# Kernel tuning notes

Hardware: AMD Instinct MI355X
Metric: run time of the kernel (lower is better)

Reference implementation:

```python
import jax, jax.numpy as jnp
import numpy as np

N = 30000      # nodes
E = 480000     # edges (before self-loops)
G = 30         # graphs
DIN = 256      # input_dim
DH = 64        # hidden_dim (per-head out channels)
H = 8          # heads in layers 0,1; last layer has 1 head


def _glorot(key, shape):
    fan_in, fan_out = shape[0], shape[-1]
    s = jnp.sqrt(2.0 / (fan_in + fan_out))
    return jax.random.normal(key, shape, dtype=jnp.float32) * s


def setup_inputs() -> dict:
    key = jax.random.key(0)
    ks = jax.random.split(key, 32)
    inp = {
        'x': jax.random.normal(ks[0], (N, DIN), dtype=jnp.float32),
        'edge_index': jax.random.randint(ks[1], (2, E), 0, N, dtype=jnp.int64),
        'batch': jnp.sort(jax.random.randint(ks[2], (N,), 0, G, dtype=jnp.int64)),
        # GAT layer 0: in=256 -> 8 heads x 64
        'W0': _glorot(ks[3], (DIN, H * DH)),
        'as0': _glorot(ks[4], (H, DH)), 'ad0': _glorot(ks[5], (H, DH)),
        'b0': jnp.zeros((H * DH,), jnp.float32),
        # GAT layer 1: in=512 -> 8 heads x 64
        'W1': _glorot(ks[6], (H * DH, H * DH)),
        'as1': _glorot(ks[7], (H, DH)), 'ad1': _glorot(ks[8], (H, DH)),
        'b1': jnp.zeros((H * DH,), jnp.float32),
        # GAT layer 2: in=512 -> 1 head x 64
        'W2': _glorot(ks[9], (H * DH, DH)),
        'as2': _glorot(ks[10], (1, DH)), 'ad2': _glorot(ks[11], (1, DH)),
        'b2': jnp.zeros((DH,), jnp.float32),
        # batch norms (feature sizes match actual activations)
        'bn0_g': jnp.ones((H * DH,), jnp.float32), 'bn0_b': jnp.zeros((H * DH,), jnp.float32),
        'bn1_g': jnp.ones((H * DH,), jnp.float32), 'bn1_b': jnp.zeros((H * DH,), jnp.float32),
        'bn2_g': jnp.ones((DH,), jnp.float32), 'bn2_b': jnp.zeros((DH,), jnp.float32),
        'ln_g': jnp.ones((DH,), jnp.float32), 'ln_b': jnp.zeros((DH,), jnp.float32),
        'fc1_w': _glorot(ks[12], (DH, DH // 2)), 'fc1_b': jnp.zeros((DH // 2,), jnp.float32),
        'fc2_w': _glorot(ks[13], (DH // 2, 2)), 'fc2_b': jnp.zeros((2,), jnp.float32),
    }
    return inp


def _gat(x, src, dst, W, a_src, a_dst, bias, heads):
    # x: [N, Fin]; project to [N, heads, DH]
    h = (x @ W).reshape(N, heads, DH)
    s_src = jnp.sum(h * a_src, axis=-1)  # [N, heads]
    s_dst = jnp.sum(h * a_dst, axis=-1)  # [N, heads]
    e = jax.nn.leaky_relu(s_src[src] + s_dst[dst], 0.2)  # [Etot, heads]
    # segment softmax over edges grouped by destination node
    m = jax.ops.segment_max(e, dst, num_segments=N)
    p = jnp.exp(e - m[dst])
    denom = jax.ops.segment_sum(p, dst, num_segments=N)
    alpha = p / (denom[dst] + 1e-16)
    out = jax.ops.segment_sum(h[src] * alpha[:, :, None], dst, num_segments=N)
    return out.reshape(N, heads * DH) + bias


def _bn(x, g, b):
    m = jnp.mean(x, axis=0)
    v = jnp.var(x, axis=0)
    return (x - m) / jnp.sqrt(v + 1e-5) * g + b


def _forward(x, edge_index, batch,
             W0, as0, ad0, b0, W1, as1, ad1, b1, W2, as2, ad2, b2,
             bn0_g, bn0_b, bn1_g, bn1_b, bn2_g, bn2_b,
             ln_g, ln_b, fc1_w, fc1_b, fc2_w, fc2_b):
    loops = jnp.arange(N, dtype=edge_index.dtype)
    src = jnp.concatenate([edge_index[0], loops])
    dst = jnp.concatenate([edge_index[1], loops])
    # layer 0: 256 -> 512; no residual (dim mismatch)
    x1 = jax.nn.elu(_bn(_gat(x, src, dst, W0, as0, ad0, b0, H), bn0_g, bn0_b))
    # layer 1: 512 -> 512; residual
    x2 = jax.nn.elu(_bn(_gat(x1, src, dst, W1, as1, ad1, b1, H), bn1_g, bn1_b)) + x1
    # layer 2 (single head): 512 -> 64; no residual
    x3 = jax.nn.elu(_bn(_gat(x2, src, dst, W2, as2, ad2, b2, 1), bn2_g, bn2_b))
    # layer norm
    mu = jnp.mean(x3, axis=-1, keepdims=True)
    var = jnp.var(x3, axis=-1, keepdims=True)
    xl = (x3 - mu) / jnp.sqrt(var + 1e-5) * ln_g + ln_b
    # global mean pool over graphs
    sums = jax.ops.segment_sum(xl, batch, num_segments=G)
    cnt = jax.ops.segment_sum(jnp.ones((N, 1), xl.dtype), batch, num_segments=G)
    pooled = sums / jnp.maximum(cnt, 1.0)
    hdd = jax.nn.elu(pooled @ fc1_w + fc1_b)
    logits = hdd @ fc2_w + fc2_b
    return jax.nn.log_softmax(logits, axis=1)


def reference(x, edge_index, batch,
              W0, as0, ad0, b0, W1, as1, ad1, b1, W2, as2, ad2, b2,
              bn0_g, bn0_b, bn1_g, bn1_b, bn2_g, bn2_b,
              ln_g, ln_b, fc1_w, fc1_b, fc2_w, fc2_b):
    return _forward(x, edge_index, batch,
                    W0, as0, ad0, b0, W1, as1, ad1, b1, W2, as2, ad2, b2,
                    bn0_g, bn0_b, bn1_g, bn1_b, bn2_g, bn2_b,
                    ln_g, ln_b, fc1_w, fc1_b, fc2_w, fc2_b)
```

## Files before the change

kernel.cpp:

```cpp
#include <hip/hip_runtime.h>
#include <math.h>

#define NODES 30000
#define NEDGE 480000
#define ETOT  (NODES + NEDGE)
#define NGRAPH 30
#define DIN 256
#define DH 64
#define CAP 128

typedef __bf16 bf16x8 __attribute__((ext_vector_type(8)));
typedef float  f32x4  __attribute__((ext_vector_type(4)));

static __device__ __forceinline__ float elu_f(float x){ return x > 0.f ? x : expm1f(x); }
static __device__ __forceinline__ float bf_lo(unsigned v){ return __uint_as_float(v << 16); }
static __device__ __forceinline__ float bf_hi(unsigned v){ return __uint_as_float(v & 0xffff0000u); }
static __device__ __forceinline__ unsigned pack_bf2(float a, float b){
  __bf16 ob[2] = {(__bf16)a, (__bf16)b};
  return *(unsigned*)ob;
}

__global__ void k_count(const int* __restrict__ ei, int* __restrict__ deg){
  int e = blockIdx.x*256 + threadIdx.x;
  if (e >= ETOT) return;
  int dst = (e < NEDGE) ? ei[NEDGE + e] : (e - NEDGE);
  atomicAdd(&deg[dst], 1);
}

__global__ void k_scan(const int* __restrict__ deg, int* __restrict__ rowptr){
  __shared__ int s[1024];
  int t = threadIdx.x;
  const int CH = (NODES + 1023) / 1024;
  int base = t * CH;
  int local = 0;
  for (int i = 0; i < CH; i++){ int idx = base + i; if (idx < NODES) local += deg[idx]; }
  s[t] = local; __syncthreads();
  for (int off = 1; off < 1024; off <<= 1){
    int v = (t >= off) ? s[t - off] : 0;
    __syncthreads();
    s[t] += v;
    __syncthreads();
  }
  int run = s[t] - local;
  for (int i = 0; i < CH; i++){
    int idx = base + i;
    if (idx < NODES){ rowptr[idx] = run; run += deg[idx]; }
  }
  if (t == 1023) rowptr[NODES] = s[1023];
}

__global__ void k_fill(const int* __restrict__ ei, const int* __restrict__ rowptr,
                       int* __restrict__ cursor, int* __restrict__ colA){
  int e = blockIdx.x*256 + threadIdx.x;
  if (e >= ETOT) return;
  int src, dst;
  if (e < NEDGE){ src = ei[e]; dst = ei[NEDGE + e]; }
  else          { src = e - NEDGE; dst = src; }
  int pos = atomicAdd(&cursor[dst], 1);
  colA[rowptr[dst] + pos] = src;
}

__global__ void k_cast4(const float* __restrict__ in, __bf16* __restrict__ out, int n4){
  int i = blockIdx.x*256 + threadIdx.x;
  if (i >= n4) return;
  float4 v = ((const float4*)in)[i];
  __bf16 o[4] = {(__bf16)v.x, (__bf16)v.y, (__bf16)v.z, (__bf16)v.w};
  *(uint2*)(out + (size_t)i*4) = *(const uint2*)o;
}

#define TW0 (512*256)
#define TW1 (512*512)
#define TW2 (64*512)
__global__ void k_transW_all(const float* __restrict__ W0, const float* __restrict__ W1,
                             const float* __restrict__ W2, __bf16* __restrict__ Wt0,
                             __bf16* __restrict__ Wt1, __bf16* __restrict__ Wt2){
  int idx = blockIdx.x*256 + threadIdx.x;
  if (idx < TW0){
    int n = idx >> 8, k = idx & 255;
    Wt0[idx] = (__bf16)W0[(size_t)k*512 + n];
  } else if (idx < TW0 + TW1){
    int j = idx - TW0;
    int n = j >> 9, k = j & 511;
    Wt1[j] = (__bf16)W1[(size_t)k*512 + n];
  } else if (idx < TW0 + TW1 + TW2){
    int j = idx - TW0 - TW1;
    int n = j >> 9, k = j & 511;
    Wt2[j] = (__bf16)W2[(size_t)k*64 + n];
  }
}

#define LSTR 72
__global__ __launch_bounds__(256) void k_gemm_bf16(const __bf16* __restrict__ A,
    const __bf16* __restrict__ Bt, __bf16* __restrict__ C,
    const float* __restrict__ asrc, const float* __restrict__ adst,
    float* __restrict__ ssrc, float* __restrict__ sdst, int heads,
    int M, int N, int K){
  __shared__ __align__(16) __bf16 As[128*LSTR];
  __shared__ __align__(16) __bf16 Bs[128*LSTR];
  int tid  = threadIdx.x;
  int lane = tid & 63, wave = tid >> 6;
  int wr = wave >> 1, wc = wave & 1;
  int q = lane >> 4, r = lane & 15;
  int rowBase = blockIdx.y * 128, colBase = blockIdx.x * 128;
  f32x4 acc[4][4] = {};
  for (int k0 = 0; k0 < K; k0 += 64){
    #pragma unroll
    for (int p = 0; p < 4; p++){
      int lin = p*256 + tid;
      int rr = lin >> 3, ko = (lin & 7) * 8;
      uint4 va = make_uint4(0,0,0,0);
      int gr = rowBase + rr;
      if (gr < M) va = *(const uint4*)(A + (size_t)gr*K + k0 + ko);
      *(uint4*)(&As[rr*LSTR + ko]) = va;
      uint4 vb = make_uint4(0,0,0,0);
      int gn = colBase + rr;
      if (gn < N) vb = *(const uint4*)(Bt + (size_t)gn*K + k0 + ko);
      *(uint4*)(&Bs[rr*LSTR + ko]) = vb;
    }
    __syncthreads();
    #pragma unroll
    for (int kk = 0; kk < 2; kk++){
      bf16x8 af[4], bfr[4];
      #pragma unroll
      for (int i = 0; i < 4; i++) af[i]  = *(const bf16x8*)(&As[(wr*64 + i*16 + r)*LSTR + kk*32 + q*8]);
      #pragma unroll
      for (int j = 0; j < 4; j++) bfr[j] = *(const bf16x8*)(&Bs[(wc*64 + j*16 + r)*LSTR + kk*32 + q*8]);
      #pragma unroll
      for (int i = 0; i < 4; i++)
        #pragma unroll
        for (int j = 0; j < 4; j++)
          acc[i][j] = __builtin_amdgcn_mfma_f32_16x16x32_bf16(af[i], bfr[j], acc[i][j], 0, 0, 0);
    }
    __syncthreads();
  }
  #pragma unroll
  for (int i = 0; i < 4; i++){
    #pragma unroll
    for (int j = 0; j < 4; j++){
      int col = colBase + wc*64 + j*16 + r;
      if (col >= N) continue;
      #pragma unroll
      for (int v = 0; v < 4; v++){
        int row = rowBase + wr*64 + i*16 + q*4 + v;
        if (row < M) C[(size_t)row*N + col] = (__bf16)acc[i][j][v];
      }
    }
  }
  int colW = colBase + wc*64;
  if (colW < N){
    int hb = colW >> 6;
    float a_s[4], a_d[4];
    #pragma unroll
    for (int j = 0; j < 4; j++){
      a_s[j] = asrc[hb*64 + j*16 + r];
      a_d[j] = adst[hb*64 + j*16 + r];
    }
    #pragma unroll
    for (int i = 0; i < 4; i++){
      #pragma unroll
      for (int v = 0; v < 4; v++){
        float s1 = 0.f, s2 = 0.f;
        #pragma unroll
        for (int j = 0; j < 4; j++){
          float av = acc[i][j][v];
          s1 += av * a_s[j];
          s2 += av * a_d[j];
        }
        #pragma unroll
        for (int off = 1; off < 16; off <<= 1){
          s1 += __shfl_xor(s1, off, 64);
          s2 += __shfl_xor(s2, off, 64);
        }
        if (r == 0){
          int row = rowBase + wr*64 + i*16 + q*4 + v;
          if (row < M){
            ssrc[(size_t)row*heads + hb] = s1;
            sdst[(size_t)row*heads + hb] = s2;
          }
        }
      }
    }
  }
}

__global__ __launch_bounds__(256) void k_gatagg8(const __bf16* __restrict__ hb,
    const float* __restrict__ ssrc, const float* __restrict__ sdst,
    const int* __restrict__ rowptr, const int* __restrict__ colA,
    const float* __restrict__ bias, __bf16* __restrict__ outb){
  int n = blockIdx.x;
  int t = threadIdx.x;
  __shared__ int ecol[CAP];
  __shared__ float p[CAP][9];
  __shared__ float dhv[8], sdsh[8], mh[8];
  int base = rowptr[n];
  int deg = rowptr[n+1] - base;
  if (t < 8) sdsh[t] = sdst[(size_t)n*8 + t];
  __syncthreads();
  int g = t >> 5, l = t & 31;
  if (deg <= CAP){
    if (t < deg){
      int c = colA[base + t];
      ecol[t] = c;
      const float4* sp = (const float4*)(ssrc + (size_t)c*8);
      float4 s0 = sp[0], s1 = sp[1];
      float v;
      v = s0.x + sdsh[0]; p[t][0] = v > 0.f ? v : 0.2f*v;
      v = s0.y + sdsh[1]; p[t][1] = v > 0.f ? v : 0.2f*v;
      v = s0.z + sdsh[2]; p[t][2] = v > 0.f ? v : 0.2f*v;
      v = s0.w + sdsh[3]; p[t][3] = v > 0.f ? v : 0.2f*v;
      v = s1.x + sdsh[4]; p[t][4] = v > 0.f ? v : 0.2f*v;
      v = s1.y + sdsh[5]; p[t][5] = v > 0.f ? v : 0.2f*v;
      v = s1.z + sdsh[6]; p[t][6] = v > 0.f ? v : 0.2f*v;
      v = s1.w + sdsh[7]; p[t][7] = v > 0.f ? v : 0.2f*v;
    }
    __syncthreads();
    {
      float m = -1e30f;
      for (int e = l; e < deg; e += 32) m = fmaxf(m, p[e][g]);
      #pragma unroll
      for (int off = 1; off < 32; off <<= 1) m = fmaxf(m, __shfl_xor(m, off, 64));
      float d = 0.f;
      for (int e = l; e < deg; e += 32){ float xv = __expf(p[e][g] - m); p[e][g] = xv; d += xv; }
      #pragma unroll
      for (int off = 1; off < 32; off <<= 1) d += __shfl_xor(d, off, 64);
      if (l == 0) dhv[g] = 1.f / (d + 1e-16f);
    }
    __syncthreads();
    int hh = g;
    float rcp = dhv[hh];
    float a0 = 0.f, a1 = 0.f, b0 = 0.f, b1 = 0.f;
    int e = 0;
    for (; e + 4 <= deg; e += 4){
      int c0 = ecol[e], c1 = ecol[e+1], c2 = ecol[e+2], c3 = ecol[e+3];
      float p0 = p[e][hh], p1 = p[e+1][hh], p2 = p[e+2][hh], p3 = p[e+3][hh];
      unsigned v0 = *(const unsigned*)(hb + (size_t)c0*512 + t*2);
      unsigned v1 = *(const unsigned*)(hb + (size_t)c1*512 + t*2);
      unsigned v2 = *(const unsigned*)(hb + (size_t)c2*512 + t*2);
      unsigned v3 = *(const unsigned*)(hb + (size_t)c3*512 + t*2);
      a0 += p0*bf_lo(v0); a1 += p0*bf_hi(v0);
      b0 += p1*bf_lo(v1); b1 += p1*bf_hi(v1);
      a0 += p2*bf_lo(v2); a1 += p2*bf_hi(v2);
      b0 += p3*bf_lo(v3); b1 += p3*bf_hi(v3);
    }
    for (; e < deg; e++){
      int c = ecol[e];
      float pe = p[e][hh];
      unsigned v = *(const unsigned*)(hb + (size_t)c*512 + t*2);
      a0 += pe*bf_lo(v); a1 += pe*bf_hi(v);
    }
    a0 += b0; a1 += b1;
    float o0 = a0*rcp + bias[t*2], o1 = a1*rcp + bias[t*2+1];
    *(unsigned*)(outb + (size_t)n*512 + t*2) = pack_bf2(o0, o1);
  } else {
    float m = -1e30f;
    for (int e = l; e < deg; e += 32){
      int c = colA[base + e];
      float sc = ssrc[(size_t)c*8 + g] + sdsh[g];
      sc = sc > 0.f ? sc : 0.2f*sc;
      m = fmaxf(m, sc);
    }
    #pragma unroll
    for (int off = 1; off < 32; off <<= 1) m = fmaxf(m, __shfl_xor(m, off, 64));
    if (l == 0) mh[g] = m;
    __syncthreads();
    float d = 0.f;
    float mm = mh[g];
    for (int e = l; e < deg; e += 32){
      int c = colA[base + e];
      float sc = ssrc[(size_t)c*8 + g] + sdsh[g];
      sc = sc > 0.f ? sc : 0.2f*sc;
      d += __expf(sc - mm);
    }
    #pragma unroll
    for (int off = 1; off < 32; off <<= 1) d += __shfl_xor(d, off, 64);
    if (l == 0) dhv[g] = 1.f / (d + 1e-16f);
    __syncthreads();
    int hh = g;
    float rcp = dhv[hh];
    float mhh = mh[hh];
    float a0 = 0.f, a1 = 0.f;
    for (int e = 0; e < deg; e++){
      int c = colA[base + e];
      float sc = ssrc[(size_t)c*8 + hh] + sdsh[hh];
      sc = sc > 0.f ? sc : 0.2f*sc;
      float pe = __expf(sc - mhh);
      unsigned v = *(const unsigned*)(hb + (size_t)c*512 + t*2);
      a0 += pe*bf_lo(v); a1 += pe*bf_hi(v);
    }
    float o0 = a0*rcp + bias[t*2], o1 = a1*rcp + bias[t*2+1];
    *(unsigned*)(outb + (size_t)n*512 + t*2) = pack_bf2(o0, o1);
  }
}

__global__ __launch_bounds__(256) void k_gatagg1(const __bf16* __restrict__ hb,
    const float* __restrict__ ssrc, const float* __restrict__ sdst,
    const int* __restrict__ rowptr, const int* __restrict__ colA,
    const float* __restrict__ bias, __bf16* __restrict__ outb){
  int n = blockIdx.x;
  int t = threadIdx.x;
  __shared__ int ecol[CAP];
  __shared__ float p[CAP];
  __shared__ float racc[8][64];
  __shared__ float dhv1, mh1, sds;
  int base = rowptr[n];
  int deg = rowptr[n+1] - base;
  if (t == 0) sds = sdst[n];
  __syncthreads();
  int g = t >> 5, l = t & 31;
  if (deg <= CAP){
    if (t < deg){
      int c = colA[base + t];
      ecol[t] = c;
      float sc = ssrc[c] + sds;
      p[t] = sc > 0.f ? sc : 0.2f*sc;
    }
    __syncthreads();
    if (t < 64){
      float m = -1e30f;
      for (int e = t; e < deg; e += 64) m = fmaxf(m, p[e]);
      #pragma unroll
      for (int off = 1; off < 64; off <<= 1) m = fmaxf(m, __shfl_xor(m, off, 64));
      float d = 0.f;
      for (int e = t; e < deg; e += 64){ float xv = __expf(p[e] - m); p[e] = xv; d += xv; }
      #pragma unroll
      for (int off = 1; off < 64; off <<= 1) d += __shfl_xor(d, off, 64);
      if (t == 0) dhv1 = 1.f / (d + 1e-16f);
    }
    __syncthreads();
    float a0 = 0.f, a1 = 0.f;
    for (int e = g; e < deg; e += 8){
      float pe = p[e];
      unsigned v = *(const unsigned*)(hb + (size_t)ecol[e]*64 + l*2);
      a0 += pe*bf_lo(v); a1 += pe*bf_hi(v);
    }
    racc[g][l*2] = a0; racc[g][l*2+1] = a1;
    __syncthreads();
    if (t < 32){
      float s0 = 0.f, s1 = 0.f;
      #pragma unroll
      for (int g2 = 0; g2 < 8; g2++){ s0 += racc[g2][t*2]; s1 += racc[g2][t*2+1]; }
      float rcp = dhv1;
      float o0 = s0*rcp + bias[t*2], o1 = s1*rcp + bias[t*2+1];
      *(unsigned*)(outb + (size_t)n*64 + t*2) = pack_bf2(o0, o1);
    }
  } else {
    if (t < 64){
      float m = -1e30f;
      for (int e = t; e < deg; e += 64){
        int c = colA[base + e];
        float sc = ssrc[c] + sds;
        sc = sc > 0.f ? sc : 0.2f*sc;
        m = fmaxf(m, sc);
      }
      #pragma unroll
      for (int off = 1; off < 64; off <<= 1) m = fmaxf(m, __shfl_xor(m, off, 64));
      if (t == 0) mh1 = m;
    }
    __syncthreads();
    if (t < 64){
      float d = 0.f;
      for (int e = t; e < deg; e += 64){
        int c = colA[base + e];
        float sc = ssrc[c] + sds;
        sc = sc > 0.f ? sc : 0.2f*sc;
        d += __expf(sc - mh1);
      }
      #pragma unroll
      for (int off = 1; off < 64; off <<= 1) d += __shfl_xor(d, off, 64);
      if (t == 0) dhv1 = 1.f / (d + 1e-16f);
    }
    __syncthreads();
    float a0 = 0.f, a1 = 0.f;
    float mm = mh1;
    for (int e = g; e < deg; e += 8){
      int c = colA[base + e];
      float sc = ssrc[c] + sds;
      sc = sc > 0.f ? sc : 0.2f*sc;
      float pe = __expf(sc - mm);
      unsigned v = *(const unsigned*)(hb + (size_t)c*64 + l*2);
      a0 += pe*bf_lo(v); a1 += pe*bf_hi(v);
    }
    racc[g][l*2] = a0; racc[g][l*2+1] = a1;
    __syncthreads();
    if (t < 32){
      float s0 = 0.f, s1 = 0.f;
      #pragma unroll
      for (int g2 = 0; g2 < 8; g2++){ s0 += racc[g2][t*2]; s1 += racc[g2][t*2+1]; }
      float rcp = dhv1;
      float o0 = s0*rcp + bias[t*2], o1 = s1*rcp + bias[t*2+1];
      *(unsigned*)(outb + (size_t)n*64 + t*2) = pack_bf2(o0, o1);
    }
  }
}

__global__ __launch_bounds__(256) void k_bnstat1(const __bf16* __restrict__ xb,
    float* __restrict__ partial, int F){
  int t = threadIdx.x;
  int OCT = F >> 3;
  int RPB = 256 / OCT;
  int o = t & (OCT - 1), r = t / OCT;
  int NB = gridDim.x;
  float s[8] = {}, q[8] = {};
  int step = NB * RPB;
  for (int n = blockIdx.x*RPB + r; n < NODES; n += step){
    uint4 v = *(const uint4*)(xb + (size_t)n*F + o*8);
    unsigned vv[4] = {v.x, v.y, v.z, v.w};
    #pragma unroll
    for (int j = 0; j < 4; j++){
      float lo = bf_lo(vv[j]), hi = bf_hi(vv[j]);
      s[2*j]   += lo; q[2*j]   += lo*lo;
      s[2*j+1] += hi; q[2*j+1] += hi*hi;
    }
  }
  __shared__ float red[256][17];
  #pragma unroll
  for (int j = 0; j < 8; j++){ red[t][j] = s[j]; red[t][8+j] = q[j]; }
  __syncthreads();
  for (int st = RPB >> 1; st > 0; st >>= 1){
    if (r < st){
      #pragma unroll
      for (int j = 0; j < 16; j++) red[t][j] += red[t + st*OCT][j];
    }
    __syncthreads();
  }
  if (r == 0){
    #pragma unroll
    for (int j = 0; j < 8; j++){
      partial[(size_t)(o*8 + j)*NB + blockIdx.x]     = red[t][j];
      partial[(size_t)(F + o*8 + j)*NB + blockIdx.x] = red[t][8 + j];
    }
  }
}

__global__ void k_bnstat2(const float* __restrict__ partial, float* __restrict__ sum,
                          float* __restrict__ sumsq, int F, int NB){
  int row = blockIdx.x;
  int t = threadIdx.x;
  float a = 0.f;
  for (int i = t; i < NB; i += 64) a += partial[(size_t)row*NB + i];
  #pragma unroll
  for (int off = 1; off < 64; off <<= 1) a += __shfl_xor(a, off, 64);
  if (t == 0){
    if (row < F) sum[row] = a;
    else         sumsq[row - F] = a;
  }
}

__global__ __launch_bounds__(256) void k_bnapply_b(const __bf16* __restrict__ xb,
    const float* __restrict__ sum, const float* __restrict__ sumsq,
    const float* __restrict__ g, const float* __restrict__ b,
    const __bf16* __restrict__ res, __bf16* __restrict__ y, int rows){
  int t = threadIdx.x;
  float2 sm = *(const float2*)(sum + t*2);
  float2 sq = *(const float2*)(sumsq + t*2);
  float2 gg = *(const float2*)(g + t*2);
  float2 bb = *(const float2*)(b + t*2);
  const float inv_n = 1.f / (float)NODES;
  float m0 = sm.x*inv_n, m1 = sm.y*inv_n;
  float v0 = sq.x*inv_n - m0*m0, v1 = sq.y*inv_n - m1*m1;
  float sc0 = gg.x * rsqrtf(v0 + 1e-5f), sc1 = gg.y * rsqrtf(v1 + 1e-5f);
  float sh0 = bb.x - m0*sc0, sh1 = bb.y - m1*sc1;
  int n0 = blockIdx.x * rows;
  for (int r = 0; r < rows; r++){
    int n = n0 + r;
    if (n >= NODES) break;
    size_t off = (size_t)n*512 + t*2;
    unsigned v = *(const unsigned*)(xb + off);
    float o0 = elu_f(bf_lo(v)*sc0 + sh0);
    float o1 = elu_f(bf_hi(v)*sc1 + sh1);
    if (res){
      unsigned rv = *(const unsigned*)(res + off);
      o0 += bf_lo(rv); o1 += bf_hi(rv);
    }
    *(unsigned*)(y + off) = pack_bf2(o0, o1);
  }
}

__global__ void k_bn_elu_ln_b(const __bf16* __restrict__ xb, const float* __restrict__ sum,
    const float* __restrict__ sumsq, const float* __restrict__ g, const float* __restrict__ b,
    const float* __restrict__ lg, const float* __restrict__ lb, float* __restrict__ y){
  int t = threadIdx.x;
  int l = t & 31, sub = t >> 5;
  int n = blockIdx.x*8 + sub;
  float2 sm = *(const float2*)(sum + l*2);
  float2 sq = *(const float2*)(sumsq + l*2);
  float2 gg = *(const float2*)(g + l*2);
  float2 bb = *(const float2*)(b + l*2);
  const float inv_n = 1.f / (float)NODES;
  float m0 = sm.x*inv_n, m1 = sm.y*inv_n;
  float va0 = sq.x*inv_n - m0*m0, va1 = sq.y*inv_n - m1*m1;
  float sc0 = gg.x * rsqrtf(va0 + 1e-5f), sc1 = gg.y * rsqrtf(va1 + 1e-5f);
  float sh0 = bb.x - m0*sc0, sh1 = bb.y - m1*sc1;
  unsigned v = *(const unsigned*)(xb + (size_t)n*64 + l*2);
  float x0 = elu_f(bf_lo(v)*sc0 + sh0);
  float x1 = elu_f(bf_hi(v)*sc1 + sh1);
  float s = x0 + x1;
  #pragma unroll
  for (int off = 1; off < 32; off <<= 1) s += __shfl_xor(s, off, 64);
  float mean = s * (1.f/64.f);
  float d0 = x0 - mean, d1 = x1 - mean;
  float qq = d0*d0 + d1*d1;
  #pragma unroll
  for (int off = 1; off < 32; off <<= 1) qq += __shfl_xor(qq, off, 64);
  float var = qq * (1.f/64.f);
  float inv = rsqrtf(var + 1e-5f);
  float2 o = make_float2(d0*inv*lg[l*2] + lb[l*2], d1*inv*lg[l*2+1] + lb[l*2+1]);
  *(float2*)(y + (size_t)n*64 + l*2) = o;
}

static __device__ int lbound(const int* a, int n, int v){
  int lo = 0, hi = n;
  while (lo < hi){ int mid = (lo + hi) >> 1; if (a[mid] < v) lo = mid + 1; else hi = mid; }
  return lo;
}

__global__ void k_pool(const float* __restrict__ xl, const int* __restrict__ batch,
                       float* __restrict__ pooled){
  int g = blockIdx.x;
  int t = threadIdx.x;
  int lo = lbound(batch, NODES, g);
  int hi = lbound(batch, NODES, g+1);
  int f = t & 63, grp = t >> 6;
  float acc = 0.f;
  for (int n = lo + grp; n < hi; n += 4) acc += xl[(size_t)n*DH + f];
  __shared__ float red[4][64];
  red[grp][f] = acc;
  __syncthreads();
  if (grp == 0){
    float s = red[0][f] + red[1][f] + red[2][f] + red[3][f];
    int cnt = hi - lo;
    pooled[g*DH + f] = s / fmaxf((float)cnt, 1.f);
  }
}

__global__ void k_head(const float* __restrict__ pooled, const float* __restrict__ w1,
                       const float* __restrict__ b1, const float* __restrict__ w2,
                       const float* __restrict__ b2, float* __restrict__ out){
  int g = threadIdx.x;
  if (g >= NGRAPH) return;
  const float* pd = pooled + g*DH;
  float hdd[32];
  for (int j = 0; j < 32; j++){
    float s = b1[j];
    for (int d = 0; d < DH; d++) s += pd[d]*w1[d*32 + j];
    hdd[j] = elu_f(s);
  }
  float l0 = b2[0], l1 = b2[1];
  for (int j = 0; j < 32; j++){ l0 += hdd[j]*w2[j*2]; l1 += hdd[j]*w2[j*2 + 1]; }
  float m = fmaxf(l0, l1);
  float lse = m + logf(expf(l0 - m) + expf(l1 - m));
  out[g*2]     = l0 - lse;
  out[g*2 + 1] = l1 - lse;
}

extern "C" void kernel_launch(void* const* d_in, const int* in_sizes, int n_in,
                              void* d_out, int out_size, void* d_ws, size_t ws_size,
                              hipStream_t stream){
  const float* x    = (const float*)d_in[0];
  const int*   ei   = (const int*)d_in[1];
  const int*   batch= (const int*)d_in[2];
  const float* W0   = (const float*)d_in[3];
  const float* as0  = (const float*)d_in[4];
  const float* ad0  = (const float*)d_in[5];
  const float* b0   = (const float*)d_in[6];
  const float* W1   = (const float*)d_in[7];
  const float* as1  = (const float*)d_in[8];
  const float* ad1  = (const float*)d_in[9];
  const float* b1   = (const float*)d_in[10];
  const float* W2   = (const float*)d_in[11];
  const float* as2  = (const float*)d_in[12];
  const float* ad2  = (const float*)d_in[13];
  const float* b2   = (const float*)d_in[14];
  const float* bn0g = (const float*)d_in[15];
  const float* bn0b = (const float*)d_in[16];
  const float* bn1g = (const float*)d_in[17];
  const float* bn1b = (const float*)d_in[18];
  const float* bn2g = (const float*)d_in[19];
  const float* bn2b = (const float*)d_in[20];
  const float* lng  = (const float*)d_in[21];
  const float* lnb  = (const float*)d_in[22];
  const float* fc1w = (const float*)d_in[23];
  const float* fc1b = (const float*)d_in[24];
  const float* fc2w = (const float*)d_in[25];
  const float* fc2b = (const float*)d_in[26];
  float* out = (float*)d_out;

  char* w = (char*)d_ws;
  auto alloc = [&](size_t bytes) -> char* {
    char* p = w; w += (bytes + 255) & ~(size_t)255; return p;
  };
  __bf16* xb0   = (__bf16*)alloc((size_t)NODES*DIN*2);
  __bf16* hbuf  = (__bf16*)alloc((size_t)NODES*512*2);
  __bf16* gbuf  = (__bf16*)alloc((size_t)NODES*512*2);
  __bf16* x1b   = (__bf16*)alloc((size_t)NODES*512*2);
  __bf16* x2b   = (__bf16*)alloc((size_t)NODES*512*2);
  __bf16* Wt0   = (__bf16*)alloc((size_t)TW0*2);
  __bf16* Wt1   = (__bf16*)alloc((size_t)TW1*2);
  __bf16* Wt2   = (__bf16*)alloc((size_t)TW2*2);
  float*  ssrc  = (float*)alloc((size_t)NODES*8*4);
  float*  sdst  = (float*)alloc((size_t)NODES*8*4);
  float*  xl    = (float*)alloc((size_t)NODES*DH*4);
  float*  pooled= (float*)alloc(NGRAPH*DH*4);
  int*    rowptr= (int*)alloc((NODES+1)*4);
  int*    colA  = (int*)alloc((size_t)ETOT*4);
  float*  partial=(float*)alloc((size_t)2*512*512*4);
  float*  sum0  = (float*)alloc(512*4);
  float*  sq0   = (float*)alloc(512*4);
  float*  sum1  = (float*)alloc(512*4);
  float*  sq1   = (float*)alloc(512*4);
  float*  sum2  = (float*)alloc(64*4);
  float*  sq2   = (float*)alloc(64*4);
  char* zbase  = w;
  int*   deg   = (int*)alloc(NODES*4);
  int*   cursor= (int*)alloc(NODES*4);
  size_t zbytes = (size_t)(w - zbase);
  hipMemsetAsync(zbase, 0, zbytes, stream);

  const int eb = (ETOT + 255)/256;
  k_count<<<eb, 256, 0, stream>>>(ei, deg);
  k_scan<<<1, 1024, 0, stream>>>(deg, rowptr);
  k_fill<<<eb, 256, 0, stream>>>(ei, rowptr, cursor, colA);

  k_cast4<<<(NODES*DIN/4 + 255)/256, 256, 0, stream>>>(x, xb0, NODES*DIN/4);
  k_transW_all<<<(TW0+TW1+TW2 + 255)/256, 256, 0, stream>>>(W0, W1, W2, Wt0, Wt1, Wt2);

  const int mb128 = (NODES + 127)/128;
  const int nb8 = (NODES + 7)/8;

  k_gemm_bf16<<<dim3(4, mb128), 256, 0, stream>>>(xb0, Wt0, hbuf, as0, ad0, ssrc, sdst, 8, NODES, 512, DIN);
  k_gatagg8<<<NODES, 256, 0, stream>>>(hbuf, ssrc, sdst, rowptr, colA, b0, gbuf);
  k_bnstat1<<<512, 256, 0, stream>>>(gbuf, partial, 512);
  k_bnstat2<<<1024, 64, 0, stream>>>(partial, sum0, sq0, 512, 512);
  k_bnapply_b<<<nb8, 256, 0, stream>>>(gbuf, sum0, sq0, bn0g, bn0b, nullptr, x1b, 8);

  k_gemm_bf16<<<dim3(4, mb128), 256, 0, stream>>>(x1b, Wt1, hbuf, as1, ad1, ssrc, sdst, 8, NODES, 512, 512);
  k_gatagg8<<<NODES, 256, 0, stream>>>(hbuf, ssrc, sdst, rowptr, colA, b1, gbuf);
  k_bnstat1<<<512, 256, 0, stream>>>(gbuf, partial, 512);
  k_bnstat2<<<1024, 64, 0, stream>>>(partial, sum1, sq1, 512, 512);
  k_bnapply_b<<<nb8, 256, 0, stream>>>(gbuf, sum1, sq1, bn1g, bn1b, x1b, x2b, 8);

  k_gemm_bf16<<<dim3(1, mb128), 256, 0, stream>>>(x2b, Wt2, hbuf, as2, ad2, ssrc, sdst, 1, NODES, 64, 512);
  k_gatagg1<<<NODES, 256, 0, stream>>>(hbuf, ssrc, sdst, rowptr, colA, b2, gbuf);
  k_bnstat1<<<256, 256, 0, stream>>>(gbuf, partial, 64);
  k_bnstat2<<<128, 64, 0, stream>>>(partial, sum2, sq2, 64, 256);
  k_bn_elu_ln_b<<<nb8, 256, 0, stream>>>(gbuf, sum2, sq2, bn2g, bn2b, lng, lnb, xl);

  k_pool<<<NGRAPH, 256, 0, stream>>>(xl, batch, pooled);
  k_head<<<1, 32, 0, stream>>>(pooled, fc1w, fc1b, fc2w, fc2b, out);
}
```

Measured before the change: 750.6 us.

## Fuse small kernels via last-block pattern and vectorize GAT aggregation

Merges count+scan, cast+weight transpose, bnstat1+bnstat2, and pool+head into single launches, using an atomic done counter so the last block finishes the reduction. This removes several launches and their inter-kernel gaps. Separately, the 8-head aggregation now has each thread load 4 bf16 features, with the two block halves taking alternate edges and combining through shared memory. The fused scan runs in one 256-thread block, and the final bnstat reduction is done serially by a single block, which may be slower than the old 1024-block reduction.

```diff
diff --git a/kernel.cpp b/kernel.cpp
--- a/kernel.cpp
+++ b/kernel.cpp
@@ -20,22 +20,27 @@
   return *(unsigned*)ob;
 }
 
-__global__ void k_count(const int* __restrict__ ei, int* __restrict__ deg){
-  int e = blockIdx.x*256 + threadIdx.x;
-  if (e >= ETOT) return;
-  int dst = (e < NEDGE) ? ei[NEDGE + e] : (e - NEDGE);
-  atomicAdd(&deg[dst], 1);
-}
-
-__global__ void k_scan(const int* __restrict__ deg, int* __restrict__ rowptr){
-  __shared__ int s[1024];
+__global__ __launch_bounds__(256) void k_countscan(const int* __restrict__ ei,
+    int* __restrict__ deg, int* __restrict__ rowptr, int* __restrict__ done){
   int t = threadIdx.x;
-  const int CH = (NODES + 1023) / 1024;
-  int base = t * CH;
+  int e = blockIdx.x*256 + t;
+  if (e < ETOT){
+    int dst = (e < NEDGE) ? ei[NEDGE + e] : (e - NEDGE);
+    atomicAdd(&deg[dst], 1);
+  }
+  __threadfence();
+  __shared__ int lastf;
+  if (t == 0) lastf = (atomicAdd(done, 1) == (int)gridDim.x - 1);
+  __syncthreads();
+  if (!lastf) return;
+  __threadfence();
+  __shared__ int s[256];
+  const int CH = (NODES + 255)/256;
+  int base = t*CH;
   int local = 0;
   for (int i = 0; i < CH; i++){ int idx = base + i; if (idx < NODES) local += deg[idx]; }
   s[t] = local; __syncthreads();
-  for (int off = 1; off < 1024; off <<= 1){
+  for (int off = 1; off < 256; off <<= 1){
     int v = (t >= off) ? s[t - off] : 0;
     __syncthreads();
     s[t] += v;
@@ -46,7 +51,7 @@
     int idx = base + i;
     if (idx < NODES){ rowptr[idx] = run; run += deg[idx]; }
   }
-  if (t == 1023) rowptr[NODES] = s[1023];
+  if (t == 255) rowptr[NODES] = s[255];
 }
 
 __global__ void k_fill(const int* __restrict__ ei, const int* __restrict__ rowptr,
@@ -60,32 +65,33 @@
   colA[rowptr[dst] + pos] = src;
 }
 
-__global__ void k_cast4(const float* __restrict__ in, __bf16* __restrict__ out, int n4){
-  int i = blockIdx.x*256 + threadIdx.x;
-  if (i >= n4) return;
-  float4 v = ((const float4*)in)[i];
-  __bf16 o[4] = {(__bf16)v.x, (__bf16)v.y, (__bf16)v.z, (__bf16)v.w};
-  *(uint2*)(out + (size_t)i*4) = *(const uint2*)o;
-}
-
+#define NCAST4 (NODES*DIN/4)
 #define TW0 (512*256)
 #define TW1 (512*512)
 #define TW2 (64*512)
-__global__ void k_transW_all(const float* __restrict__ W0, const float* __restrict__ W1,
-                             const float* __restrict__ W2, __bf16* __restrict__ Wt0,
-                             __bf16* __restrict__ Wt1, __bf16* __restrict__ Wt2){
+__global__ void k_prep(const float* __restrict__ x, __bf16* __restrict__ xb0,
+                       const float* __restrict__ W0, const float* __restrict__ W1,
+                       const float* __restrict__ W2, __bf16* __restrict__ Wt0,
+                       __bf16* __restrict__ Wt1, __bf16* __restrict__ Wt2){
   int idx = blockIdx.x*256 + threadIdx.x;
-  if (idx < TW0){
-    int n = idx >> 8, k = idx & 255;
-    Wt0[idx] = (__bf16)W0[(size_t)k*512 + n];
-  } else if (idx < TW0 + TW1){
-    int j = idx - TW0;
-    int n = j >> 9, k = j & 511;
-    Wt1[j] = (__bf16)W1[(size_t)k*512 + n];
-  } else if (idx < TW0 + TW1 + TW2){
-    int j = idx - TW0 - TW1;
-    int n = j >> 9, k = j & 511;
-    Wt2[j] = (__bf16)W2[(size_t)k*64 + n];
+  if (idx < NCAST4){
+    float4 v = ((const float4*)x)[idx];
+    __bf16 o[4] = {(__bf16)v.x, (__bf16)v.y, (__bf16)v.z, (__bf16)v.w};
+    *(uint2*)(xb0 + (size_t)idx*4) = *(const uint2*)o;
+    return;
+  }
+  int j = idx - NCAST4;
+  if (j < TW0){
+    int n = j >> 8, k = j & 255;
+    Wt0[j] = (__bf16)W0[(size_t)k*512 + n];
+  } else if (j < TW0 + TW1){
+    int j1 = j - TW0;
+    int n = j1 >> 9, k = j1 & 511;
+    Wt1[j1] = (__bf16)W1[(size_t)k*512 + n];
+  } else if (j < TW0 + TW1 + TW2){
+    int j2 = j - TW0 - TW1;
+    int n = j2 >> 9, k = j2 & 511;
+    Wt2[j2] = (__bf16)W2[(size_t)k*64 + n];
   }
 }
 
@@ -191,12 +197,17 @@
   int t = threadIdx.x;
   __shared__ int ecol[CAP];
   __shared__ float p[CAP][9];
+  __shared__ float racc[512];
   __shared__ float dhv[8], sdsh[8], mh[8];
   int base = rowptr[n];
   int deg = rowptr[n+1] - base;
   if (t < 8) sdsh[t] = sdst[(size_t)n*8 + t];
   __syncthreads();
   int g = t >> 5, l = t & 31;
+  int half = t >> 7;
+  int tf = t & 127;
+  int f4 = tf * 4;
+  int hh4 = tf >> 4;
   if (deg <= CAP){
     if (t < deg){
       int c = colA[base + t];
@@ -226,31 +237,38 @@
       if (l == 0) dhv[g] = 1.f / (d + 1e-16f);
     }
     __syncthreads();
-    int hh = g;
-    float rcp = dhv[hh];
-    float a0 = 0.f, a1 = 0.f, b0 = 0.f, b1 = 0.f;
-    int e = 0;
-    for (; e + 4 <= deg; e += 4){
-      int c0 = ecol[e], c1 = ecol[e+1], c2 = ecol[e+2], c3 = ecol[e+3];
-      float p0 = p[e][hh], p1 = p[e+1][hh], p2 = p[e+2][hh], p3 = p[e+3][hh];
-      unsigned v0 = *(const unsigned*)(hb + (size_t)c0*512 + t*2);
-      unsigned v1 = *(const unsigned*)(hb + (size_t)c1*512 + t*2);
-      unsigned v2 = *(const unsigned*)(hb + (size_t)c2*512 + t*2);
-      unsigned v3 = *(const unsigned*)(hb + (size_t)c3*512 + t*2);
-      a0 += p0*bf_lo(v0); a1 += p0*bf_hi(v0);
-      b0 += p1*bf_lo(v1); b1 += p1*bf_hi(v1);
-      a0 += p2*bf_lo(v2); a1 += p2*bf_hi(v2);
-      b0 += p3*bf_lo(v3); b1 += p3*bf_hi(v3);
-    }
-    for (; e < deg; e++){
+    float4 a = make_float4(0.f, 0.f, 0.f, 0.f);
+    int e = half;
+    for (; e + 2 < deg; e += 4){
+      int c0 = ecol[e], c1 = ecol[e+2];
+      float p0 = p[e][hh4], p1 = p[e+2][hh4];
+      uint2 v0 = *(const uint2*)(hb + (size_t)c0*512 + f4);
+      uint2 v1 = *(const uint2*)(hb + (size_t)c1*512 + f4);
+      a.x += p0*bf_lo(v0.x); a.y += p0*bf_hi(v0.x);
+      a.z += p0*bf_lo(v0.y); a.w += p0*bf_hi(v0.y);
+      a.x += p1*bf_lo(v1.x); a.y += p1*bf_hi(v1.x);
+      a.z += p1*bf_lo(v1.y); a.w += p1*bf_hi(v1.y);
+    }
+    for (; e < deg; e += 2){
       int c = ecol[e];
-      float pe = p[e][hh];
-      unsigned v = *(const unsigned*)(hb + (size_t)c*512 + t*2);
-      a0 += pe*bf_lo(v); a1 += pe*bf_hi(v);
-    }
-    a0 += b0; a1 += b1;
-    float o0 = a0*rcp + bias[t*2], o1 = a1*rcp + bias[t*2+1];
-    *(unsigned*)(outb + (size_t)n*512 + t*2) = pack_bf2(o0, o1);
+      float pe = p[e][hh4];
+      uint2 v = *(const uint2*)(hb + (size_t)c*512 + f4);
+      a.x += pe*bf_lo(v.x); a.y += pe*bf_hi(v.x);
+      a.z += pe*bf_lo(v.y); a.w += pe*bf_hi(v.y);
+    }
+    if (half == 1) *(float4*)&racc[f4] = a;
+    __syncthreads();
+    if (half == 0){
+      float4 o = *(const float4*)&racc[f4];
+      float rcp = dhv[hh4];
+      float4 bb = *(const float4*)(bias + f4);
+      float r0 = (a.x + o.x)*rcp + bb.x;
+      float r1 = (a.y + o.y)*rcp + bb.y;
+      float r2 = (a.z + o.z)*rcp + bb.z;
+      float r3 = (a.w + o.w)*rcp + bb.w;
+      uint2 st; st.x = pack_bf2(r0, r1); st.y = pack_bf2(r2, r3);
+      *(uint2*)(outb + (size_t)n*512 + f4) = st;
+    }
   } else {
     float m = -1e30f;
     for (int e = l; e < deg; e += 32){
@@ -275,20 +293,31 @@
     for (int off = 1; off < 32; off <<= 1) d += __shfl_xor(d, off, 64);
     if (l == 0) dhv[g] = 1.f / (d + 1e-16f);
     __syncthreads();
-    int hh = g;
-    float rcp = dhv[hh];
-    float mhh = mh[hh];
-    float a0 = 0.f, a1 = 0.f;
-    for (int e = 0; e < deg; e++){
+    float4 a = make_float4(0.f, 0.f, 0.f, 0.f);
+    float mhh = mh[hh4];
+    float sdd = sdsh[hh4];
+    for (int e = half; e < deg; e += 2){
       int c = colA[base + e];
-      float sc = ssrc[(size_t)c*8 + hh] + sdsh[hh];
+      float sc = ssrc[(size_t)c*8 + hh4] + sdd;
       sc = sc > 0.f ? sc : 0.2f*sc;
       float pe = __expf(sc - mhh);
-      unsigned v = *(const unsigned*)(hb + (size_t)c*512 + t*2);
-      a0 += pe*bf_lo(v); a1 += pe*bf_hi(v);
-    }
-    float o0 = a0*rcp + bias[t*2], o1 = a1*rcp + bias[t*2+1];
-    *(unsigned*)(outb + (size_t)n*512 + t*2) = pack_bf2(o0, o1);
+      uint2 v = *(const uint2*)(hb + (size_t)c*512 + f4);
+      a.x += pe*bf_lo(v.x); a.y += pe*bf_hi(v.x);
+      a.z += pe*bf_lo(v.y); a.w += pe*bf_hi(v.y);
+    }
+    if (half == 1) *(float4*)&racc[f4] = a;
+    __syncthreads();
+    if (half == 0){
+      float4 o = *(const float4*)&racc[f4];
+      float rcp = dhv[hh4];
+      float4 bb = *(const float4*)(bias + f4);
+      float r0 = (a.x + o.x)*rcp + bb.x;
+      float r1 = (a.y + o.y)*rcp + bb.y;
+      float r2 = (a.z + o.z)*rcp + bb.z;
+      float r3 = (a.w + o.w)*rcp + bb.w;
+      uint2 st; st.x = pack_bf2(r0, r1); st.y = pack_bf2(r2, r3);
+      *(uint2*)(outb + (size_t)n*512 + f4) = st;
+    }
   }
 }
 
@@ -393,8 +422,9 @@
   }
 }
 
-__global__ __launch_bounds__(256) void k_bnstat1(const __bf16* __restrict__ xb,
-    float* __restrict__ partial, int F){
+__global__ __launch_bounds__(256) void k_bnstat(const __bf16* __restrict__ xb,
+    float* __restrict__ partial, float* __restrict__ sum, float* __restrict__ sumsq,
+    int F, int* __restrict__ done){
   int t = threadIdx.x;
   int OCT = F >> 3;
   int RPB = 256 / OCT;
@@ -430,19 +460,19 @@
       partial[(size_t)(F + o*8 + j)*NB + blockIdx.x] = red[t][8 + j];
     }
   }
-}
-
-__global__ void k_bnstat2(const float* __restrict__ partial, float* __restrict__ sum,
-                          float* __restrict__ sumsq, int F, int NB){
-  int row = blockIdx.x;
-  int t = threadIdx.x;
-  float a = 0.f;
-  for (int i = t; i < NB; i += 64) a += partial[(size_t)row*NB + i];
-  #pragma unroll
-  for (int off = 1; off < 64; off <<= 1) a += __shfl_xor(a, off, 64);
-  if (t == 0){
-    if (row < F) sum[row] = a;
-    else         sumsq[row - F] = a;
+  __threadfence();
+  __shared__ int lastf;
+  if (t == 0) lastf = (atomicAdd(done, 1) == NB - 1);
+  __syncthreads();
+  if (!lastf) return;
+  __threadfence();
+  int rows = 2*F;
+  int nb4 = NB >> 2;
+  for (int row = t; row < rows; row += 256){
+    const float4* pr = (const float4*)(partial + (size_t)row*NB);
+    float a = 0.f;
+    for (int i = 0; i < nb4; i++){ float4 v = pr[i]; a += (v.x + v.y) + (v.z + v.w); }
+    if (row < F) sum[row] = a; else sumsq[row - F] = a;
   }
 }
 
@@ -514,8 +544,11 @@
   return lo;
 }
 
-__global__ void k_pool(const float* __restrict__ xl, const int* __restrict__ batch,
-                       float* __restrict__ pooled){
+__global__ __launch_bounds__(256) void k_poolhead(const float* __restrict__ xl,
+    const int* __restrict__ batch, float* __restrict__ pooled,
+    const float* __restrict__ w1, const float* __restrict__ b1,
+    const float* __restrict__ w2, const float* __restrict__ b2,
+    float* __restrict__ out, int* __restrict__ done){
   int g = blockIdx.x;
   int t = threadIdx.x;
   int lo = lbound(batch, NODES, g);
@@ -531,14 +564,14 @@
     int cnt = hi - lo;
     pooled[g*DH + f] = s / fmaxf((float)cnt, 1.f);
   }
-}
-
-__global__ void k_head(const float* __restrict__ pooled, const float* __restrict__ w1,
-                       const float* __restrict__ b1, const float* __restrict__ w2,
-                       const float* __restrict__ b2, float* __restrict__ out){
-  int g = threadIdx.x;
-  if (g >= NGRAPH) return;
-  const float* pd = pooled + g*DH;
+  __threadfence();
+  __shared__ int lastf;
+  if (t == 0) lastf = (atomicAdd(done, 1) == NGRAPH - 1);
+  __syncthreads();
+  if (!lastf) return;
+  __threadfence();
+  if (t >= NGRAPH) return;
+  const float* pd = pooled + t*DH;
   float hdd[32];
   for (int j = 0; j < 32; j++){
     float s = b1[j];
@@ -549,8 +582,8 @@
   for (int j = 0; j < 32; j++){ l0 += hdd[j]*w2[j*2]; l1 += hdd[j]*w2[j*2 + 1]; }
   float m = fmaxf(l0, l1);
   float lse = m + logf(expf(l0 - m) + expf(l1 - m));
-  out[g*2]     = l0 - lse;
-  out[g*2 + 1] = l1 - lse;
+  out[t*2]     = l0 - lse;
+  out[t*2 + 1] = l1 - lse;
 }
 
 extern "C" void kernel_launch(void* const* d_in, const int* in_sizes, int n_in,
@@ -613,38 +646,34 @@
   char* zbase  = w;
   int*   deg   = (int*)alloc(NODES*4);
   int*   cursor= (int*)alloc(NODES*4);
+  int*   dones = (int*)alloc(8*4);
   size_t zbytes = (size_t)(w - zbase);
   hipMemsetAsync(zbase, 0, zbytes, stream);
 
   const int eb = (ETOT + 255)/256;
-  k_count<<<eb, 256, 0, stream>>>(ei, deg);
-  k_scan<<<1, 1024, 0, stream>>>(deg, rowptr);
+  k_countscan<<<eb, 256, 0, stream>>>(ei, deg, rowptr, &dones[0]);
   k_fill<<<eb, 256, 0, stream>>>(ei, rowptr, cursor, colA);
 
-  k_cast4<<<(NODES*DIN/4 + 255)/256, 256, 0, stream>>>(x, xb0, NODES*DIN/4);
-  k_transW_all<<<(TW0+TW1+TW2 + 255)/256, 256, 0, stream>>>(W0, W1, W2, Wt0, Wt1, Wt2);
+  const int prep_total = NCAST4 + TW0 + TW1 + TW2;
+  k_prep<<<(prep_total + 255)/256, 256, 0, stream>>>(x, xb0, W0, W1, W2, Wt0, Wt1, Wt2);
 
   const int mb128 = (NODES + 127)/128;
   const int nb8 = (NODES + 7)/8;
 
   k_gemm_bf16<<<dim3(4, mb128), 256, 0, stream>>>(xb0, Wt0, hbuf, as0, ad0, ssrc, sdst, 8, NODES, 512, DIN);
   k_gatagg8<<<NODES, 256, 0, stream>>>(hbuf, ssrc, sdst, rowptr, colA, b0, gbuf);
-  k_bnstat1<<<512, 256, 0, stream>>>(gbuf, partial, 512);
-  k_bnstat2<<<1024, 64, 0, stream>>>(partial, sum0, sq0, 512, 512);
+  k_bnstat<<<512, 256, 0, stream>>>(gbuf, partial, sum0, sq0, 512, &dones[1]);
   k_bnapply_b<<<nb8, 256, 0, stream>>>(gbuf, sum0, sq0, bn0g, bn0b, nullptr, x1b, 8);
 
   k_gemm_bf16<<<dim3(4, mb128), 256, 0, stream>>>(x1b, Wt1, hbuf, as1, ad1, ssrc, sdst, 8, NODES, 512, 512);
   k_gatagg8<<<NODES, 256, 0, stream>>>(hbuf, ssrc, sdst, rowptr, colA, b1, gbuf);
-  k_bnstat1<<<512, 256, 0, stream>>>(gbuf, partial, 512);
-  k_bnstat2<<<1024, 64, 0, stream>>>(partial, sum1, sq1, 512, 512);
+  k_bnstat<<<512, 256, 0, stream>>>(gbuf, partial, sum1, sq1, 512, &dones[2]);
   k_bnapply_b<<<nb8, 256, 0, stream>>>(gbuf, sum1, sq1, bn1g, bn1b, x1b, x2b, 8);
 
   k_gemm_bf16<<<dim3(1, mb128), 256, 0, stream>>>(x2b, Wt2, hbuf, as2, ad2, ssrc, sdst, 1, NODES, 64, 512);
   k_gatagg1<<<NODES, 256, 0, stream>>>(hbuf, ssrc, sdst, rowptr, colA, b2, gbuf);
-  k_bnstat1<<<256, 256, 0, stream>>>(gbuf, partial, 64);
-  k_bnstat2<<<128, 64, 0, stream>>>(partial, sum2, sq2, 64, 256);
+  k_bnstat<<<256, 256, 0, stream>>>(gbuf, partial, sum2, sq2, 64, &dones[3]);
   k_bn_elu_ln_b<<<nb8, 256, 0, stream>>>(gbuf, sum2, sq2, bn2g, bn2b, lng, lnb, xl);
 
-  k_pool<<<NGRAPH, 256, 0, stream>>>(xl, batch, pooled);
-  k_head<<<1, 32, 0, stream>>>(pooled, fc1w, fc1b, fc2w, fc2b, out);
-}
+  k_poolhead<<<NGRAPH, 256, 0, stream>>>(xl, batch, pooled, fc1w, fc1b, fc2w, fc2b, out, &dones[4]);
+}
```

Result: slower. 1.174 ms (+56.5%).
